# Performance work log

Measured on AMD Instinct MI355X. Metric: run time of the kernel, lower is better.

## Reference

```python
import jax, jax.numpy as jnp
import numpy as np

EPS = 1e-12
LORA_RANK = 16

def setup_inputs() -> dict:
    key = jax.random.key(0)
    ks = jax.random.split(key, 7)
    bs, sq, din, dout = 8, 2048, 2048, 2048
    n_tasks, n_splits, n_skills, r = 32, 1, 8, LORA_RANK
    return {
        'x': jax.random.normal(ks[0], (bs, sq, din), dtype=jnp.float32),
        'W': jax.random.normal(ks[1], (dout, din), dtype=jnp.float32) * (1.0 / np.sqrt(din)),
        'b': jax.random.normal(ks[2], (dout,), dtype=jnp.float32) * 0.02,
        'module_logits': jax.random.normal(ks[3], (n_tasks, n_splits * n_skills), dtype=jnp.float32) * 0.001,
        'A': jax.random.normal(ks[4], (n_splits, n_skills, din // n_splits, r), dtype=jnp.float32) * 0.02,
        'B': jax.random.normal(ks[5], (n_splits, n_skills, r, dout // n_splits), dtype=jnp.float32) * 0.02,
        'tasks': jax.random.randint(ks[6], (bs,), 0, n_tasks),
    }

def reference(x, W, b, module_logits, A, B, tasks):
    bs, sq, din = x.shape
    n_splits, n_skills, _, r = A.shape
    dout = W.shape[0]
    # Polytropon selector (eval mode): sigmoid + normalize over skills
    probs = jax.nn.sigmoid(module_logits[tasks]).reshape(bs, n_splits, n_skills)
    probs = probs / (probs.sum(-1, keepdims=True) + EPS)  # [bs, p, t]
    # WeightedSum combinor: per-example skill mixture of LoRA params
    A_c = jnp.einsum('bpt,ptir->bpir', probs, A)  # [bs, p, din/p, r]
    B_c = jnp.einsum('bpt,ptro->bpro', probs, B)  # [bs, p, r, dout/p]
    # LoRA forward: reshape to per-example [din, r] and [r, dout]
    A_r = A_c.reshape(bs, din, r)
    B_r = jnp.transpose(B_c, (0, 2, 1, 3)).reshape(bs, r, dout)
    lora = jnp.einsum('bsr,bro->bso', jnp.einsum('bsi,bir->bsr', x, A_r), B_r)
    base = jnp.einsum('bsi,oi->bso', x, W) + b
    return base + lora * (1.0 / r)
```

## Files before the change

### kernel.cpp

```cpp
#include <hip/hip_runtime.h>

typedef __attribute__((ext_vector_type(4))) float f32x4;
typedef __attribute__((ext_vector_type(8))) short bf16x8;

__device__ __forceinline__ unsigned short f2b(float f) {
  unsigned u = __float_as_uint(f);
  u = (u + 0x7FFFu + ((u >> 16) & 1u)) >> 16;
  return (unsigned short)u;
}

#define BAR() asm volatile("s_barrier" ::: "memory")
#define VMCNT(N) asm volatile("s_waitcnt vmcnt(" #N ")" ::: "memory")

__global__ void combine_kernel(const float* __restrict__ logits,
                               const int*   __restrict__ tasks,
                               const float* __restrict__ A,
                               const float* __restrict__ B,
                               unsigned short* __restrict__ Art,
                               unsigned short* __restrict__ Brt)
{
  int idx = blockIdx.x * 256 + threadIdx.x;
  int b = idx >> 11;
  int i = idx & 2047;
  if (b >= 8) return;
  int task = tasks[b];
  float p[8]; float s = 0.f;
  #pragma unroll
  for (int t = 0; t < 8; ++t) {
    float l = logits[task * 8 + t];
    float e = 1.f / (1.f + __expf(-l));
    p[t] = e; s += e;
  }
  float inv = 1.f / (s + 1e-12f);
  #pragma unroll
  for (int t = 0; t < 8; ++t) p[t] *= inv;

  float ar[16];
  #pragma unroll
  for (int r = 0; r < 16; ++r) ar[r] = 0.f;
  for (int t = 0; t < 8; ++t) {
    const float* ap = A + ((size_t)t * 2048 + i) * 16;
    float pt = p[t];
    #pragma unroll
    for (int r = 0; r < 16; ++r) ar[r] += pt * ap[r];
  }
  #pragma unroll
  for (int r = 0; r < 16; ++r)
    Art[((size_t)b * 16 + r) * 2048 + i] = f2b(ar[r]);

  float br[16];
  #pragma unroll
  for (int r = 0; r < 16; ++r) br[r] = 0.f;
  for (int t = 0; t < 8; ++t) {
    float pt = p[t];
    #pragma unroll
    for (int r = 0; r < 16; ++r) br[r] += pt * B[((size_t)t * 16 + r) * 2048 + i];
  }
  #pragma unroll
  for (int r = 0; r < 16; ++r)
    Brt[((size_t)b * 2048 + i) * 16 + r] = f2b(br[r] * 0.0625f);
}

__global__ void prep_kernel(const float* __restrict__ x,
                            const unsigned short* __restrict__ Art,
                            const float* __restrict__ W,
                            unsigned short* __restrict__ Wb,
                            unsigned short* __restrict__ xb,
                            unsigned short* __restrict__ xa)
{
  __shared__ float red[4][16][16];
  int blk = blockIdx.x;
  int tid = threadIdx.x;
  if (blk >= 1024) {
    int idx0 = (blk - 1024) * 256 + tid;
    #pragma unroll
    for (int c = 0; c < 32; ++c) {
      size_t i = ((size_t)idx0 + (size_t)c * 32768) * 4;
      f32x4 v = *(const f32x4*)(W + i);
      ushort4 o;
      o.x = f2b(v.x); o.y = f2b(v.y); o.z = f2b(v.z); o.w = f2b(v.w);
      *(ushort4*)(Wb + i) = o;
    }
    return;
  }
  int lane = tid & 63, wv = tid >> 6;
  int lr = lane & 15, hi = lane >> 4;
  int rowbase = blk * 16;
  int batch = rowbase >> 11;
  int row = rowbase + lr;
  f32x4 acc; acc.x = 0.f; acc.y = 0.f; acc.z = 0.f; acc.w = 0.f;
  const float* xrow = x + (size_t)row * 2048 + wv * 512 + hi * 8;
  unsigned short* xbrow = xb + (size_t)row * 2048 + wv * 512 + hi * 8;
  const unsigned short* artrow = Art + ((size_t)batch * 16 + lr) * 2048 + wv * 512 + hi * 8;
  #pragma unroll
  for (int ks = 0; ks < 16; ++ks) {
    f32x4 v0 = *(const f32x4*)(xrow + ks * 32);
    f32x4 v1 = *(const f32x4*)(xrow + ks * 32 + 4);
    bf16x8 av;
    av[0] = (short)f2b(v0.x); av[1] = (short)f2b(v0.y);
    av[2] = (short)f2b(v0.z); av[3] = (short)f2b(v0.w);
    av[4] = (short)f2b(v1.x); av[5] = (short)f2b(v1.y);
    av[6] = (short)f2b(v1.z); av[7] = (short)f2b(v1.w);
    *(bf16x8*)(xbrow + ks * 32) = av;
    bf16x8 bv = *(const bf16x8*)(artrow + ks * 32);
    acc = __builtin_amdgcn_mfma_f32_16x16x32_bf16(av, bv, acc, 0, 0, 0);
  }
  #pragma unroll
  for (int j = 0; j < 4; ++j) red[wv][hi * 4 + j][lr] = acc[j];
  __syncthreads();
  int rr = tid >> 4, cc = tid & 15;
  float s = red[0][rr][cc] + red[1][rr][cc] + red[2][rr][cc] + red[3][rr][cc];
  xa[(size_t)(rowbase + rr) * 16 + cc] = f2b(s);
}

__global__ __launch_bounds__(512, 2)
void gemm_kernel(const unsigned short* __restrict__ xb,
                 const unsigned short* __restrict__ Wb,
                 const float* __restrict__ bias,
                 const unsigned short* __restrict__ xa,
                 const unsigned short* __restrict__ Brt,
                 float* __restrict__ out)
{
  __shared__ __align__(16) char lds[131072];
  const int tid = threadIdx.x;
  const int lane = tid & 63;
  const int wv = tid >> 6;
  const int wr = wv >> 2, wc = wv & 3;
  const int lr = lane & 15, hi = lane >> 4;
  const int hi16 = hi * 16;

  const int bid = blockIdx.x;
  const int swz = (bid & 7) * 64 + (bid >> 3);
  const int tm = swz >> 3, tn = swz & 7;
  const int rowbase = tm * 256, colbase = tn * 256;

  const int row0 = tid >> 3;
  const int cb0 = (tid & 7) * 16;
  const int scb_e = (cb0 ^ ((row0 & 7) << 4)) >> 1;
  const int rb5 = ((row0 >> 5) << 6) + (row0 & 31);

#define GL16(LDSOFF, GPTR) \
  __builtin_amdgcn_global_load_lds((const __attribute__((address_space(1))) unsigned int*)(GPTR), \
      (__attribute__((address_space(3))) unsigned int*)(lds + (LDSOFF)), 16, 0, 0)

#define STAGE_A(MH, DBUF, KOFF) { \
  const unsigned short* g_ = xb + (size_t)(rowbase + (MH)*64 + row0) * 2048 + (KOFF) + scb_e; \
  GL16((DBUF)*65536 + (MH)*16384 + tid*16, g_); \
  GL16((DBUF)*65536 + (MH)*16384 + 8192 + tid*16, g_ + 128*2048); \
}
#define STAGE_B(NH, DBUF, KOFF) { \
  const unsigned short* g_ = Wb + (size_t)(colbase + (NH)*32 + rb5) * 2048 + (KOFF) + scb_e; \
  GL16((DBUF)*65536 + 32768 + (NH)*16384 + tid*16, g_); \
  GL16((DBUF)*65536 + 32768 + (NH)*16384 + 8192 + tid*16, g_ + 128*2048); \
}

#define READ_A(MH) \
  _Pragma("unroll") \
  for (int mf = 0; mf < 4; ++mf) { \
    int ar_ = (MH)*128 + wr*64 + mf*16 + lr; \
    _Pragma("unroll") \
    for (int kk = 0; kk < 2; ++kk) \
      a[mf][kk] = *(const bf16x8*)(Ab + ar_*128 + ((kk*64 + hi16) ^ ((ar_&7)<<4))); \
  }
#define READ_B(NH, BREG) \
  _Pragma("unroll") \
  for (int nf = 0; nf < 2; ++nf) { \
    int br_ = (NH)*128 + wc*32 + nf*16 + lr; \
    _Pragma("unroll") \
    for (int kk = 0; kk < 2; ++kk) \
      BREG[nf][kk] = *(const bf16x8*)(Bb + br_*128 + ((kk*64 + hi16) ^ ((br_&7)<<4))); \
  }
#define MFMA_BLOCK(MH, NH, BREG) \
  __builtin_amdgcn_s_setprio(1); \
  _Pragma("unroll") \
  for (int mf = 0; mf < 4; ++mf) \
    _Pragma("unroll") \
    for (int nf = 0; nf < 2; ++nf) \
      _Pragma("unroll") \
      for (int kk = 0; kk < 2; ++kk) \
        acc[(MH)*4+mf][(NH)*2+nf] = __builtin_amdgcn_mfma_f32_16x16x32_bf16( \
            a[mf][kk], BREG[nf][kk], acc[(MH)*4+mf][(NH)*2+nf], 0, 0, 0); \
  __builtin_amdgcn_s_setprio(0);

  f32x4 acc[8][4];
  #pragma unroll
  for (int i = 0; i < 8; ++i)
    #pragma unroll
    for (int n = 0; n < 4; ++n) { acc[i][n].x = 0.f; acc[i][n].y = 0.f; acc[i][n].z = 0.f; acc[i][n].w = 0.f; }

  bf16x8 a[4][2], b0[2][2], b1[2][2];

  STAGE_A(0, 0, 0);
  STAGE_B(0, 0, 0);
  STAGE_A(1, 0, 0);
  STAGE_B(1, 0, 0);
  STAGE_A(0, 1, 64);
  STAGE_B(0, 1, 64);
  VMCNT(8);
  BAR();

  for (int kt = 0; kt < 32; ++kt) {
    const int buf = kt & 1, nbuf = buf ^ 1;
    const char* Ab = lds + buf * 65536;
    const char* Bb = Ab + 32768;
    const int k1 = (kt + 1) * 64, k2 = (kt + 2) * 64;

    READ_A(0);
    READ_B(0, b0);
    if (kt < 31) STAGE_A(1, nbuf, k1);
    BAR();
    MFMA_BLOCK(0, 0, b0);
    if (kt < 31) { VMCNT(6); } else { VMCNT(0); }
    BAR();

    READ_B(1, b1);
    if (kt < 31) STAGE_B(1, nbuf, k1);
    BAR();
    MFMA_BLOCK(0, 1, b1);
    BAR();

    READ_A(1);
    if (kt < 30) STAGE_A(0, buf, k2);
    BAR();
    MFMA_BLOCK(1, 0, b0);
    BAR();

    if (kt < 30) STAGE_B(0, buf, k2);
    BAR();
    MFMA_BLOCK(1, 1, b1);
    if (kt < 30) { VMCNT(6); }
    else if (kt == 30) { VMCNT(4); }
    BAR();
  }

  const int batch = rowbase >> 11;
  bf16x8 zf = (bf16x8)(short)0;
  bf16x8 av[8], bv[4];
  #pragma unroll
  for (int i = 0; i < 8; ++i) {
    if (hi < 2)
      av[i] = *(const bf16x8*)(xa + (size_t)(rowbase + wr * 128 + i * 16 + lr) * 16 + hi * 8);
    else
      av[i] = zf;
  }
  #pragma unroll
  for (int n = 0; n < 4; ++n) {
    if (hi < 2)
      bv[n] = *(const bf16x8*)(Brt + ((size_t)batch * 2048 + colbase + wc * 64 + n * 16 + lr) * 16 + hi * 8);
    else
      bv[n] = zf;
  }
  #pragma unroll
  for (int i = 0; i < 8; ++i)
    #pragma unroll
    for (int n = 0; n < 4; ++n)
      acc[i][n] = __builtin_amdgcn_mfma_f32_16x16x32_bf16(av[i], bv[n], acc[i][n], 0, 0, 0);

  #pragma unroll
  for (int n = 0; n < 4; ++n) {
    int col = colbase + wc * 64 + n * 16 + lr;
    float bbv = bias[col];
    #pragma unroll
    for (int i = 0; i < 8; ++i) {
      int r0 = rowbase + wr * 128 + i * 16 + hi * 4;
      #pragma unroll
      for (int j = 0; j < 4; ++j)
        out[(size_t)(r0 + j) * 2048 + col] = acc[i][n][j] + bbv;
    }
  }
#undef GL16
#undef STAGE_A
#undef STAGE_B
#undef READ_A
#undef READ_B
#undef MFMA_BLOCK
}

extern "C" void kernel_launch(void* const* d_in, const int* in_sizes, int n_in,
                              void* d_out, int out_size, void* d_ws, size_t ws_size,
                              hipStream_t stream) {
  const float* x      = (const float*)d_in[0];
  const float* W      = (const float*)d_in[1];
  const float* bias   = (const float*)d_in[2];
  const float* logits = (const float*)d_in[3];
  const float* A      = (const float*)d_in[4];
  const float* B      = (const float*)d_in[5];
  const int*   tasks  = (const int*)d_in[6];
  float* out = (float*)d_out;

  char* ws = (char*)d_ws;
  unsigned short* xb  = (unsigned short*)(ws);
  unsigned short* Wb  = (unsigned short*)(ws + 67108864);
  unsigned short* xa  = (unsigned short*)(ws + 67108864 + 8388608);
  unsigned short* Art = (unsigned short*)(ws + 67108864 + 8388608 + 524288);
  unsigned short* Brt = (unsigned short*)(ws + 67108864 + 8388608 + 1048576);

  combine_kernel<<<64, 256, 0, stream>>>(logits, tasks, A, B, Art, Brt);
  prep_kernel<<<1152, 256, 0, stream>>>(x, Art, W, Wb, xb, xa);
  gemm_kernel<<<512, 512, 0, stream>>>(xb, Wb, bias, xa, Brt, out);
}
```

Measured before the change: 193.3 us.

## Restructure GEMM main loop into finer-grained staged pipeline with explicit LDS waits

Rewrites the bf16 GEMM main loop as a two-k-tile iteration. Each quarter-tile load of A or B is issued right after the matching LDS region has been consumed, so the full next buffer is prefetched ahead rather than only part of it. It adds explicit lgkmcnt(0) waits with sched barriers before each MFMA block and changes the row-to-tile mapping of the A and B staging, with matching epilogue index remapping. The goal is deeper overlap of global-to-LDS traffic with MFMA work. The trade-off is more barriers and scheduling constraints that may stall waves.

```diff
diff --git a/kernel.cpp b/kernel.cpp
--- a/kernel.cpp
+++ b/kernel.cpp
@@ -11,6 +11,7 @@
 
 #define BAR() asm volatile("s_barrier" ::: "memory")
 #define VMCNT(N) asm volatile("s_waitcnt vmcnt(" #N ")" ::: "memory")
+#define LGKM0() { asm volatile("s_waitcnt lgkmcnt(0)" ::: "memory"); __builtin_amdgcn_sched_barrier(0); }
 
 __global__ void combine_kernel(const float* __restrict__ logits,
                                const int*   __restrict__ tasks,
@@ -134,43 +135,51 @@
   const int tm = swz >> 3, tn = swz & 7;
   const int rowbase = tm * 256, colbase = tn * 256;
 
-  const int row0 = tid >> 3;
-  const int cb0 = (tid & 7) * 16;
-  const int scb_e = (cb0 ^ ((row0 & 7) << 4)) >> 1;
-  const int rb5 = ((row0 >> 5) << 6) + (row0 & 31);
+  const int l0 = tid >> 3,          cb0 = (tid & 7) * 16;
+  const int l1 = (tid + 512) >> 3,  cb1 = ((tid + 512) & 7) * 16;
+  const int sc0 = (cb0 ^ ((l0 & 7) << 4)) >> 1;
+  const int sc1 = (cb1 ^ ((l1 & 7) << 4)) >> 1;
+  const int arow0 = ((l0 >> 6) << 7) + (l0 & 63);
+  const int arow1 = ((l1 >> 6) << 7) + (l1 & 63);
+  const int brow0 = ((l0 >> 5) << 6) + (l0 & 31);
+  const int brow1 = ((l1 >> 5) << 6) + (l1 & 31);
 
 #define GL16(LDSOFF, GPTR) \
   __builtin_amdgcn_global_load_lds((const __attribute__((address_space(1))) unsigned int*)(GPTR), \
       (__attribute__((address_space(3))) unsigned int*)(lds + (LDSOFF)), 16, 0, 0)
 
-#define STAGE_A(MH, DBUF, KOFF) { \
-  const unsigned short* g_ = xb + (size_t)(rowbase + (MH)*64 + row0) * 2048 + (KOFF) + scb_e; \
-  GL16((DBUF)*65536 + (MH)*16384 + tid*16, g_); \
-  GL16((DBUF)*65536 + (MH)*16384 + 8192 + tid*16, g_ + 128*2048); \
-}
-#define STAGE_B(NH, DBUF, KOFF) { \
-  const unsigned short* g_ = Wb + (size_t)(colbase + (NH)*32 + rb5) * 2048 + (KOFF) + scb_e; \
-  GL16((DBUF)*65536 + 32768 + (NH)*16384 + tid*16, g_); \
-  GL16((DBUF)*65536 + 32768 + (NH)*16384 + 8192 + tid*16, g_ + 128*2048); \
-}
-
-#define READ_A(MH) \
+#define STAGE_A(H, DBUF, KO) { \
+  GL16((DBUF)*65536 + (H)*16384 + tid*16, \
+       xb + (size_t)(rowbase + arow0 + (H)*64) * 2048 + (KO) + sc0); \
+  GL16((DBUF)*65536 + (H)*16384 + 8192 + tid*16, \
+       xb + (size_t)(rowbase + arow1 + (H)*64) * 2048 + (KO) + sc1); \
+}
+#define STAGE_B(H, DBUF, KO) { \
+  GL16((DBUF)*65536 + 32768 + (H)*16384 + tid*16, \
+       Wb + (size_t)(colbase + brow0 + (H)*32) * 2048 + (KO) + sc0); \
+  GL16((DBUF)*65536 + 32768 + (H)*16384 + 8192 + tid*16, \
+       Wb + (size_t)(colbase + brow1 + (H)*32) * 2048 + (KO) + sc1); \
+}
+
+#define RD_A(H, BUF) \
   _Pragma("unroll") \
   for (int mf = 0; mf < 4; ++mf) { \
-    int ar_ = (MH)*128 + wr*64 + mf*16 + lr; \
+    int lrw_ = wr*64 + mf*16 + lr; \
     _Pragma("unroll") \
     for (int kk = 0; kk < 2; ++kk) \
-      a[mf][kk] = *(const bf16x8*)(Ab + ar_*128 + ((kk*64 + hi16) ^ ((ar_&7)<<4))); \
-  }
-#define READ_B(NH, BREG) \
+      a[mf][kk] = *(const bf16x8*)(lds + (BUF)*65536 + (H)*16384 + lrw_*128 + \
+                                   ((kk*64 + hi16) ^ ((lrw_&7)<<4))); \
+  }
+#define RD_B(H, BUF, BREG) \
   _Pragma("unroll") \
   for (int nf = 0; nf < 2; ++nf) { \
-    int br_ = (NH)*128 + wc*32 + nf*16 + lr; \
+    int lrw_ = wc*32 + nf*16 + lr; \
     _Pragma("unroll") \
     for (int kk = 0; kk < 2; ++kk) \
-      BREG[nf][kk] = *(const bf16x8*)(Bb + br_*128 + ((kk*64 + hi16) ^ ((br_&7)<<4))); \
-  }
-#define MFMA_BLOCK(MH, NH, BREG) \
+      BREG[nf][kk] = *(const bf16x8*)(lds + (BUF)*65536 + 32768 + (H)*16384 + lrw_*128 + \
+                                      ((kk*64 + hi16) ^ ((lrw_&7)<<4))); \
+  }
+#define MM(H, BH, BREG) \
   __builtin_amdgcn_s_setprio(1); \
   _Pragma("unroll") \
   for (int mf = 0; mf < 4; ++mf) \
@@ -178,8 +187,8 @@
     for (int nf = 0; nf < 2; ++nf) \
       _Pragma("unroll") \
       for (int kk = 0; kk < 2; ++kk) \
-        acc[(MH)*4+mf][(NH)*2+nf] = __builtin_amdgcn_mfma_f32_16x16x32_bf16( \
-            a[mf][kk], BREG[nf][kk], acc[(MH)*4+mf][(NH)*2+nf], 0, 0, 0); \
+        acc[(H)*4+mf][(BH)*2+nf] = __builtin_amdgcn_mfma_f32_16x16x32_bf16( \
+            a[mf][kk], BREG[nf][kk], acc[(H)*4+mf][(BH)*2+nf], 0, 0, 0); \
   __builtin_amdgcn_s_setprio(0);
 
   f32x4 acc[8][4];
@@ -190,79 +199,89 @@
 
   bf16x8 a[4][2], b0[2][2], b1[2][2];
 
-  STAGE_A(0, 0, 0);
-  STAGE_B(0, 0, 0);
-  STAGE_A(1, 0, 0);
-  STAGE_B(1, 0, 0);
-  STAGE_A(0, 1, 64);
-  STAGE_B(0, 1, 64);
-  VMCNT(8);
+  STAGE_B(0, 0, 0);  STAGE_A(0, 0, 0);  STAGE_B(1, 0, 0);  STAGE_A(1, 0, 0);
+  STAGE_B(0, 1, 64); STAGE_A(0, 1, 64); STAGE_B(1, 1, 64); STAGE_A(1, 1, 64);
+  VMCNT(6);
   BAR();
-
-  for (int kt = 0; kt < 32; ++kt) {
-    const int buf = kt & 1, nbuf = buf ^ 1;
-    const char* Ab = lds + buf * 65536;
-    const char* Bb = Ab + 32768;
-    const int k1 = (kt + 1) * 64, k2 = (kt + 2) * 64;
-
-    READ_A(0);
-    READ_B(0, b0);
-    if (kt < 31) STAGE_A(1, nbuf, k1);
-    BAR();
-    MFMA_BLOCK(0, 0, b0);
-    if (kt < 31) { VMCNT(6); } else { VMCNT(0); }
-    BAR();
-
-    READ_B(1, b1);
-    if (kt < 31) STAGE_B(1, nbuf, k1);
-    BAR();
-    MFMA_BLOCK(0, 1, b1);
-    BAR();
-
-    READ_A(1);
-    if (kt < 30) STAGE_A(0, buf, k2);
-    BAR();
-    MFMA_BLOCK(1, 0, b0);
-    BAR();
-
-    if (kt < 30) STAGE_B(0, buf, k2);
-    BAR();
-    MFMA_BLOCK(1, 1, b1);
-    if (kt < 30) { VMCNT(6); }
-    else if (kt == 30) { VMCNT(4); }
+  RD_B(0, 0, b0);
+
+  for (int it = 0; it < 16; ++it) {
+    const int koe = (2 * it + 2) * 64, koo = (2 * it + 3) * 64;
+    const bool st = (it < 15);
+
+    RD_A(0, 0);
+    if (st) STAGE_B(0, 0, koe);
+    BAR(); LGKM0();
+    MM(0, 0, b0);
+    BAR();
+    RD_B(1, 0, b1);
+    if (st) STAGE_A(0, 0, koe);
+    BAR(); LGKM0();
+    MM(0, 1, b1);
+    BAR();
+    RD_A(1, 0);
+    if (st) STAGE_B(1, 0, koe);
+    BAR(); LGKM0();
+    MM(1, 0, b0);
+    BAR();
+    if (st) { STAGE_A(1, 0, koe); VMCNT(6); } else { VMCNT(0); }
+    RD_B(0, 1, b0);
+    BAR(); LGKM0();
+    MM(1, 1, b1);
+    BAR();
+    RD_A(0, 1);
+    if (st) STAGE_B(0, 1, koo);
+    BAR(); LGKM0();
+    MM(0, 0, b0);
+    BAR();
+    RD_B(1, 1, b1);
+    if (st) STAGE_A(0, 1, koo);
+    BAR(); LGKM0();
+    MM(0, 1, b1);
+    BAR();
+    RD_A(1, 1);
+    if (st) STAGE_B(1, 1, koo);
+    BAR(); LGKM0();
+    MM(1, 0, b0);
+    BAR();
+    if (st) { STAGE_A(1, 1, koo); VMCNT(6); RD_B(0, 0, b0); }
+    BAR(); LGKM0();
+    MM(1, 1, b1);
     BAR();
   }
 
   const int batch = rowbase >> 11;
   bf16x8 zf = (bf16x8)(short)0;
-  bf16x8 av[8], bv[4];
+  bf16x8 ea[8], eb[4];
   #pragma unroll
   for (int i = 0; i < 8; ++i) {
+    int trow = wr * 128 + (i >> 2) * 64 + (i & 3) * 16 + lr;
     if (hi < 2)
-      av[i] = *(const bf16x8*)(xa + (size_t)(rowbase + wr * 128 + i * 16 + lr) * 16 + hi * 8);
+      ea[i] = *(const bf16x8*)(xa + (size_t)(rowbase + trow) * 16 + hi * 8);
     else
-      av[i] = zf;
+      ea[i] = zf;
   }
   #pragma unroll
   for (int n = 0; n < 4; ++n) {
+    int tcol = wc * 64 + (n >> 1) * 32 + (n & 1) * 16 + lr;
     if (hi < 2)
-      bv[n] = *(const bf16x8*)(Brt + ((size_t)batch * 2048 + colbase + wc * 64 + n * 16 + lr) * 16 + hi * 8);
+      eb[n] = *(const bf16x8*)(Brt + ((size_t)batch * 2048 + colbase + tcol) * 16 + hi * 8);
     else
-      bv[n] = zf;
+      eb[n] = zf;
   }
   #pragma unroll
   for (int i = 0; i < 8; ++i)
     #pragma unroll
     for (int n = 0; n < 4; ++n)
-      acc[i][n] = __builtin_amdgcn_mfma_f32_16x16x32_bf16(av[i], bv[n], acc[i][n], 0, 0, 0);
+      acc[i][n] = __builtin_amdgcn_mfma_f32_16x16x32_bf16(ea[i], eb[n], acc[i][n], 0, 0, 0);
 
   #pragma unroll
   for (int n = 0; n < 4; ++n) {
-    int col = colbase + wc * 64 + n * 16 + lr;
+    int col = colbase + wc * 64 + (n >> 1) * 32 + (n & 1) * 16 + lr;
     float bbv = bias[col];
     #pragma unroll
     for (int i = 0; i < 8; ++i) {
-      int r0 = rowbase + wr * 128 + i * 16 + hi * 4;
+      int r0 = rowbase + wr * 128 + (i >> 2) * 64 + (i & 3) * 16 + hi * 4;
       #pragma unroll
       for (int j = 0; j < 4; ++j)
         out[(size_t)(r0 + j) * 2048 + col] = acc[i][n][j] + bbv;
@@ -271,9 +290,9 @@
 #undef GL16
 #undef STAGE_A
 #undef STAGE_B
-#undef READ_A
-#undef READ_B
-#undef MFMA_BLOCK
+#undef RD_A
+#undef RD_B
+#undef MM
 }
 
 extern "C" void kernel_launch(void* const* d_in, const int* in_sizes, int n_in,
```

New measurement: 190.9 us. About the same (-1.2%).
